# Optimization experiments

Measured on AMD Instinct MI355X. Metric: run time of the kernel, lower is better.

## Reference

```python
import jax, jax.numpy as jnp
import numpy as np

N_CLASSES = 100
MAX_POSSIBLE = 8.0
A, B, C_COEF = 1.0, 0.1, 0.0


def setup_inputs() -> dict:
    key = jax.random.key(0)
    k1, k2 = jax.random.split(key)
    pred = jax.random.normal(k1, (2000000, 64), dtype=jnp.float32)
    group_idx = jax.random.randint(k2, (2000000,), 0, N_CLASSES, dtype=jnp.int64)
    return {"pred": pred, "group_idx": group_idx}


def reference(pred, group_idx):
    C = N_CLASSES
    idx = group_idx.astype(jnp.int32)
    ones = jnp.ones((pred.shape[0],), dtype=pred.dtype)
    counts = jax.ops.segment_sum(ones, idx, num_segments=C)          # [C]
    s = jax.ops.segment_sum(pred, idx, num_segments=C)               # [C, D]
    sq = jax.ops.segment_sum(pred * pred, idx, num_segments=C)       # [C, D]
    cnt = counts[:, None]
    mean = s / cnt                                                   # [C, D]
    # unbiased variance (torch .std default ddof=1)
    var = (sq - cnt * mean * mean) / (cnt - 1.0)
    std = jnp.sqrt(jnp.maximum(var, 0.0))                            # [C, D]

    cov = jnp.sum(jnp.sum(std, axis=0) ** 2) / C

    # pairwise squared distances between class means, [C, C]
    gram = mean @ mean.T
    norms = jnp.diagonal(gram)
    dist = norms[:, None] + norms[None, :] - 2.0 * gram
    pair_mask = jnp.tril(jnp.ones((C, C), dtype=bool), k=-1)         # i > j pairs
    n_pairs = C * (C - 1) / 2.0
    mean_distance = jnp.sum(jnp.where(pair_mask, dist, 0.0)) / n_pairs
    min_dist = jnp.min(jnp.where(pair_mask, dist, jnp.inf))

    loss = (A * cov
            + B * (MAX_POSSIBLE - mean_distance) ** 2
            + C_COEF * (MAX_POSSIBLE - min_dist) ** 2)
    return (loss, mean_distance, min_dist, cov)
```

## Files before the change

### kernel.cpp

```cpp
#include <hip/hip_runtime.h>
#include <math.h>

#define NCLS 100
#define D 64
#define GACC_FLOATS (NCLS * D * 2 + NCLS)
#define G1 512
#define BLK 256
#define PBLK 12800
#define SUPF 8192

typedef __attribute__((ext_vector_type(8)))  short bf16x8;
typedef __attribute__((ext_vector_type(16))) float f32x16;

#define ZV16 {0.f,0.f,0.f,0.f,0.f,0.f,0.f,0.f,0.f,0.f,0.f,0.f,0.f,0.f,0.f,0.f}

union B8 { uint32_t u[4]; bf16x8 v; };

__device__ __forceinline__ uint32_t cvtpk(float lo, float hi) {
    uint32_t r;
    asm("v_cvt_pk_bf16_f32 %0, %1, %2" : "=v"(r) : "v"(lo), "v"(hi));
    return r;
}

__device__ __forceinline__ void global_fadd(float* p, float v) {
    asm volatile("global_atomic_add_f32 %0, %1, off"
                 :: "v"((uint64_t)(uintptr_t)p), "v"(v));
}

__device__ __forceinline__ void lds_fadd(uint32_t byteoff, float v) {
    asm volatile("ds_add_f32 %0, %1" :: "v"(byteoff), "v"(v));
}

struct IdxRegs { int4 a, b, c, d; };

__device__ __forceinline__ IdxRegs load_idx(const int* __restrict__ idx, size_t mtile, int kg) {
    const int* p = idx + mtile * 32 + (size_t)kg * 8;
    IdxRegs r;
    r.a = *(const int4*)p;        r.b = *(const int4*)(p + 4);
    r.c = *(const int4*)(p + 16); r.d = *(const int4*)(p + 20);
    return r;
}

__device__ __forceinline__ void stage_super(const float* __restrict__ pred, size_t st,
                                            float* buf, int w, int lane) {
    const float* src = pred + st * SUPF;
    #pragma unroll
    for (int r = 0; r < 8; ++r) {
        int c = r * 4 + w;
        const float* gs = src + (size_t)c * 256 + (size_t)lane * 4;
        float* ls = buf + c * 256;
        __builtin_amdgcn_global_load_lds(
            (const __attribute__((address_space(1))) uint32_t*)gs,
            (__attribute__((address_space(3))) uint32_t*)ls, 16, 0, 0);
    }
}

__global__ __launch_bounds__(BLK) void seg_mfma_kernel(
    const float* __restrict__ pred, const int* __restrict__ idx,
    float* __restrict__ part, float* __restrict__ gacc,
    int nrows, int atomicPath)
{
    __shared__ float sbuf[2][SUPF];

    const int bid   = blockIdx.x;
    const int tid   = threadIdx.x;
    const int lane  = tid & 63;
    const int w     = tid >> 6;
    const int col   = lane & 31;
    const int kg    = lane >> 5;
    const int mycls = w * 32 + col;

    f32x16 aS0 = ZV16, aS1 = ZV16, aQ0 = ZV16, aQ1 = ZV16;

    const size_t nst = (size_t)nrows >> 7;
    const size_t st0 = (size_t)bid * nst / G1;
    const size_t st1 = ((size_t)bid + 1) * nst / G1;

    if (st0 < st1) {
        stage_super(pred, st0, sbuf[0], w, lane);
        IdxRegs ir = load_idx(idx, st0 * 4, kg);
        __syncthreads();

        int cur = 0;
        for (size_t st = st0; st < st1; ++st) {
            if (st + 1 < st1)
                stage_super(pred, st + 1, sbuf[cur ^ 1], w, lane);

            #pragma unroll
            for (int mt = 0; mt < 4; ++mt) {
                size_t nmt = st * 4 + mt + 1;
                IdxRegs irn = (nmt < st1 * 4) ? load_idx(idx, nmt, kg) : ir;

                const float* pb = sbuf[cur] + mt * 2048;
                #pragma unroll
                for (int kk = 0; kk < 2; ++kk) {
                    const int4 i0 = kk ? ir.c : ir.a;
                    const int4 i1 = kk ? ir.d : ir.b;
                    B8 ab;
                    ab.u[0] = cvtpk(i0.x==mycls?1.f:0.f, i0.y==mycls?1.f:0.f);
                    ab.u[1] = cvtpk(i0.z==mycls?1.f:0.f, i0.w==mycls?1.f:0.f);
                    ab.u[2] = cvtpk(i1.x==mycls?1.f:0.f, i1.y==mycls?1.f:0.f);
                    ab.u[3] = cvtpk(i1.z==mycls?1.f:0.f, i1.w==mycls?1.f:0.f);

                    const float* base = pb + (kk * 16 + kg * 8) * 64 + col;
                    #pragma unroll
                    for (int n = 0; n < 2; ++n) {
                        float v[8];
                        #pragma unroll
                        for (int e = 0; e < 8; ++e) v[e] = base[e * 64 + n * 32];
                        B8 bv, bq;
                        #pragma unroll
                        for (int e = 0; e < 4; ++e) {
                            bv.u[e] = cvtpk(v[2*e],         v[2*e+1]);
                            bq.u[e] = cvtpk(v[2*e]*v[2*e],  v[2*e+1]*v[2*e+1]);
                        }
                        if (n == 0) {
                            aS0 = __builtin_amdgcn_mfma_f32_32x32x16_bf16(ab.v, bv.v, aS0, 0, 0, 0);
                            aQ0 = __builtin_amdgcn_mfma_f32_32x32x16_bf16(ab.v, bq.v, aQ0, 0, 0, 0);
                        } else {
                            aS1 = __builtin_amdgcn_mfma_f32_32x32x16_bf16(ab.v, bv.v, aS1, 0, 0, 0);
                            aQ1 = __builtin_amdgcn_mfma_f32_32x32x16_bf16(ab.v, bq.v, aQ1, 0, 0, 0);
                        }
                    }
                }
                ir = irn;
            }
            __syncthreads();
            cur ^= 1;
        }
    }

    if (bid == 0 && (nrows & 127)) {
        for (size_t base = nst * 128; base < (size_t)nrows; base += 16) {
            int c[8]; float v0[8], v1[8];
            #pragma unroll
            for (int e = 0; e < 8; ++e) {
                size_t kk = base + (size_t)kg * 8 + e;
                bool ok = kk < (size_t)nrows;
                c[e]  = ok ? idx[kk] : -1;
                v0[e] = ok ? pred[kk * 64 + col] : 0.0f;
                v1[e] = ok ? pred[kk * 64 + 32 + col] : 0.0f;
            }
            B8 ab, b0, q0, b1, q1;
            #pragma unroll
            for (int e = 0; e < 4; ++e) {
                ab.u[e] = cvtpk(c[2*e]==mycls?1.f:0.f, c[2*e+1]==mycls?1.f:0.f);
                b0.u[e] = cvtpk(v0[2*e],          v0[2*e+1]);
                q0.u[e] = cvtpk(v0[2*e]*v0[2*e],  v0[2*e+1]*v0[2*e+1]);
                b1.u[e] = cvtpk(v1[2*e],          v1[2*e+1]);
                q1.u[e] = cvtpk(v1[2*e]*v1[2*e],  v1[2*e+1]*v1[2*e+1]);
            }
            aS0 = __builtin_amdgcn_mfma_f32_32x32x16_bf16(ab.v, b0.v, aS0, 0, 0, 0);
            aQ0 = __builtin_amdgcn_mfma_f32_32x32x16_bf16(ab.v, q0.v, aQ0, 0, 0, 0);
            aS1 = __builtin_amdgcn_mfma_f32_32x32x16_bf16(ab.v, b1.v, aS1, 0, 0, 0);
            aQ1 = __builtin_amdgcn_mfma_f32_32x32x16_bf16(ab.v, q1.v, aQ1, 0, 0, 0);
        }
    }

    if (!atomicPath) {
        float* pp = part + (size_t)bid * PBLK;
        #pragma unroll
        for (int reg = 0; reg < 16; ++reg) {
            int row = (reg & 3) + 8 * (reg >> 2) + 4 * kg;
            int gm  = w * 32 + row;
            if (gm < NCLS) {
                pp[gm * 64 + col]              = aS0[reg];
                pp[gm * 64 + 32 + col]         = aS1[reg];
                pp[6400 + gm * 64 + col]       = aQ0[reg];
                pp[6400 + gm * 64 + 32 + col]  = aQ1[reg];
            }
        }
    } else {
        #pragma unroll
        for (int reg = 0; reg < 16; ++reg) {
            int row = (reg & 3) + 8 * (reg >> 2) + 4 * kg;
            int gm  = w * 32 + row;
            if (gm < NCLS) {
                global_fadd(&gacc[gm * 64 + col],             aS0[reg]);
                global_fadd(&gacc[gm * 64 + 32 + col],        aS1[reg]);
                global_fadd(&gacc[6400 + gm * 64 + col],      aQ0[reg]);
                global_fadd(&gacc[6400 + gm * 64 + 32 + col], aQ1[reg]);
            }
        }
    }
}

__global__ __launch_bounds__(256) void hist_kernel(
    const int* __restrict__ idx, float* __restrict__ gcnt, int nrows)
{
    __shared__ uint32_t hh[NCLS];
    for (int i = threadIdx.x; i < NCLS; i += 256) hh[i] = 0u;
    __syncthreads();

    const int tid = blockIdx.x * 256 + threadIdx.x;
    const int stride = gridDim.x * 256;
    const int n4 = nrows >> 2;
    for (int i = tid; i < n4; i += stride) {
        int4 c = ((const int4*)idx)[i];
        atomicAdd(&hh[c.x], 1u); atomicAdd(&hh[c.y], 1u);
        atomicAdd(&hh[c.z], 1u); atomicAdd(&hh[c.w], 1u);
    }
    for (int i = (n4 << 2) + tid; i < nrows; i += stride)
        atomicAdd(&hh[idx[i]], 1u);
    __syncthreads();

    for (int i = threadIdx.x; i < NCLS; i += 256)
        if (hh[i]) global_fadd(&gcnt[i], (float)hh[i]);
}

__global__ __launch_bounds__(256) void reduce_kernel(
    const float* __restrict__ part, float* __restrict__ gacc)
{
    int pos = blockIdx.x * 256 + threadIdx.x;
    if (pos >= PBLK) return;
    const int bq = G1 / 8;
    int b0 = blockIdx.y * bq;

    const float* p = part + (size_t)b0 * PBLK + pos;
    float s0 = 0.f, s1 = 0.f, s2 = 0.f, s3 = 0.f;
    #pragma unroll 1
    for (int b = 0; b + 4 <= bq; b += 4) {
        s0 += p[(size_t)(b + 0) * PBLK];
        s1 += p[(size_t)(b + 1) * PBLK];
        s2 += p[(size_t)(b + 2) * PBLK];
        s3 += p[(size_t)(b + 3) * PBLK];
    }
    global_fadd(&gacc[pos], (s0 + s1) + (s2 + s3));
}

#define MSTR 68

__global__ __launch_bounds__(1024) void finalize_kernel(
    const float* __restrict__ gacc, float* __restrict__ out)
{
    __shared__ float mean_s[NCLS * MSTR];
    __shared__ float colstd[D];
    __shared__ float norms[NCLS];
    __shared__ float redSum[16], redMin[16];
    __shared__ float s_cov;

    const float* gSum = gacc;
    const float* gSq  = gacc + NCLS * D;
    const float* gCnt = gacc + 2 * NCLS * D;

    for (int d = threadIdx.x; d < D; d += 1024) colstd[d] = 0.0f;
    __syncthreads();

    for (int i = threadIdx.x; i < NCLS * D; i += 1024) {
        int c = i >> 6, d = i & 63;
        float cnt = gCnt[c];
        float m   = gSum[i] / cnt;
        float var = (gSq[i] - cnt * m * m) / (cnt - 1.0f);
        float sd  = sqrtf(fmaxf(var, 0.0f));
        mean_s[c * MSTR + d] = m;
        lds_fadd((uint32_t)(uintptr_t)(&colstd[d]), sd);
    }
    asm volatile("s_waitcnt lgkmcnt(0)" ::: "memory");
    __syncthreads();

    if (threadIdx.x < 64) {
        float v = colstd[threadIdx.x];
        v = v * v;
        for (int o = 32; o; o >>= 1) v += __shfl_down(v, o);
        if (threadIdx.x == 0) s_cov = v / (float)NCLS;
    }

    for (int c = threadIdx.x; c < NCLS; c += 1024) {
        const float4* mp = (const float4*)&mean_s[c * MSTR];
        float n = 0.0f;
        #pragma unroll
        for (int d4 = 0; d4 < D / 4; ++d4) {
            float4 a = mp[d4];
            n += a.x * a.x + a.y * a.y + a.z * a.z + a.w * a.w;
        }
        norms[c] = n;
    }
    __syncthreads();

    const int n_pairs = NCLS * (NCLS - 1) / 2;
    float lsum = 0.0f, lmin = INFINITY;
    for (int p = threadIdx.x; p < n_pairs; p += 1024) {
        int i = (int)((1.0f + sqrtf(1.0f + 8.0f * (float)p)) * 0.5f);
        while (i * (i - 1) / 2 > p) --i;
        while ((i + 1) * i / 2 <= p) ++i;
        int j = p - i * (i - 1) / 2;

        const float4* mi = (const float4*)&mean_s[i * MSTR];
        const float4* mj = (const float4*)&mean_s[j * MSTR];
        float dot = 0.0f;
        #pragma unroll
        for (int d4 = 0; d4 < D / 4; ++d4) {
            float4 a = mi[d4], b = mj[d4];
            dot += a.x * b.x + a.y * b.y + a.z * b.z + a.w * b.w;
        }
        float dist = norms[i] + norms[j] - 2.0f * dot;
        lsum += dist;
        lmin = fminf(lmin, dist);
    }

    for (int o = 32; o; o >>= 1) {
        lsum += __shfl_down(lsum, o);
        lmin = fminf(lmin, __shfl_down(lmin, o));
    }
    int ww = threadIdx.x >> 6;
    if ((threadIdx.x & 63) == 0) { redSum[ww] = lsum; redMin[ww] = lmin; }
    __syncthreads();

    if (threadIdx.x == 0) {
        float S = 0.0f, M = INFINITY;
        for (int k = 0; k < 16; ++k) { S += redSum[k]; M = fminf(M, redMin[k]); }
        float md  = S / (float)n_pairs;
        float cov = s_cov;
        float e   = 8.0f - md;
        float loss = 1.0f * cov + 0.1f * e * e;
        out[0] = loss;
        out[1] = md;
        out[2] = M;
        out[3] = cov;
    }
}

extern "C" void kernel_launch(void* const* d_in, const int* in_sizes, int n_in,
                              void* d_out, int out_size, void* d_ws, size_t ws_size,
                              hipStream_t stream) {
    const float* pred = (const float*)d_in[0];
    const int*   gidx = (const int*)d_in[1];
    float* out = (float*)d_out;
    int nrows = in_sizes[1];

    const size_t partFloats = (size_t)G1 * PBLK;

    if (ws_size >= (partFloats + GACC_FLOATS) * sizeof(float)) {
        float* part = (float*)d_ws;
        float* gacc = part + partFloats;
        hipMemsetAsync(gacc, 0, GACC_FLOATS * sizeof(float), stream);
        seg_mfma_kernel<<<G1, BLK, 0, stream>>>(pred, gidx, part, gacc, nrows, 0);
        hist_kernel<<<1024, 256, 0, stream>>>(gidx, gacc + 2 * NCLS * D, nrows);
        dim3 gridR((PBLK + 255) / 256, 8);
        reduce_kernel<<<gridR, 256, 0, stream>>>(part, gacc);
        finalize_kernel<<<1, 1024, 0, stream>>>(gacc, out);
    } else {
        float* gacc = (float*)d_ws;
        hipMemsetAsync(gacc, 0, GACC_FLOATS * sizeof(float), stream);
        seg_mfma_kernel<<<G1, BLK, 0, stream>>>(pred, gidx, nullptr, gacc, nrows, 1);
        hist_kernel<<<1024, 256, 0, stream>>>(gidx, gacc + 2 * NCLS * D, nrows);
        finalize_kernel<<<1, 1024, 0, stream>>>(gacc, out);
    }
}
```

Before: 189.0 us.

## Stage indices through LDS and hand-schedule async loads with explicit waitcnt

Group-index loads move from per-thread global reads into the same async global-to-LDS staging path as pred. The main loop uses explicit vmcnt waits, raw s_barrier and inline-asm ds_read2/ds_read_b128 fetches. The super-tile is halved and the grid doubled, with launch bounds of four blocks per CU, so more blocks stay resident while memory traffic overlaps with MFMA work. The vmcnt(5) count assumes exactly five outstanding loads per stage and the asm LDS addressing is hand-computed, so any mismatch in either would silently corrupt results.

```diff
diff --git a/kernel.cpp b/kernel.cpp
--- a/kernel.cpp
+++ b/kernel.cpp
@@ -4,13 +4,15 @@
 #define NCLS 100
 #define D 64
 #define GACC_FLOATS (NCLS * D * 2 + NCLS)
-#define G1 512
+#define G1 1024
 #define BLK 256
 #define PBLK 12800
-#define SUPF 8192
+#define SUPF 4096
 
 typedef __attribute__((ext_vector_type(8)))  short bf16x8;
 typedef __attribute__((ext_vector_type(16))) float f32x16;
+typedef __attribute__((ext_vector_type(2)))  float f32x2;
+typedef __attribute__((ext_vector_type(4)))  int   i32x4;
 
 #define ZV16 {0.f,0.f,0.f,0.f,0.f,0.f,0.f,0.f,0.f,0.f,0.f,0.f,0.f,0.f,0.f,0.f}
 
@@ -31,36 +33,32 @@
     asm volatile("ds_add_f32 %0, %1" :: "v"(byteoff), "v"(v));
 }
 
-struct IdxRegs { int4 a, b, c, d; };
-
-__device__ __forceinline__ IdxRegs load_idx(const int* __restrict__ idx, size_t mtile, int kg) {
-    const int* p = idx + mtile * 32 + (size_t)kg * 8;
-    IdxRegs r;
-    r.a = *(const int4*)p;        r.b = *(const int4*)(p + 4);
-    r.c = *(const int4*)(p + 16); r.d = *(const int4*)(p + 20);
-    return r;
-}
-
-__device__ __forceinline__ void stage_super(const float* __restrict__ pred, size_t st,
-                                            float* buf, int w, int lane) {
+__device__ __forceinline__ void stage_super(const float* __restrict__ pred,
+                                            const int* __restrict__ idx, size_t st,
+                                            float* sb, int* ib, int w, int lane) {
     const float* src = pred + st * SUPF;
     #pragma unroll
-    for (int r = 0; r < 8; ++r) {
+    for (int r = 0; r < 4; ++r) {
         int c = r * 4 + w;
         const float* gs = src + (size_t)c * 256 + (size_t)lane * 4;
-        float* ls = buf + c * 256;
+        float* ls = sb + c * 256;
         __builtin_amdgcn_global_load_lds(
             (const __attribute__((address_space(1))) uint32_t*)gs,
             (__attribute__((address_space(3))) uint32_t*)ls, 16, 0, 0);
     }
-}
-
-__global__ __launch_bounds__(BLK) void seg_mfma_kernel(
+    const int* gi = idx + st * 64 + lane;
+    __builtin_amdgcn_global_load_lds(
+        (const __attribute__((address_space(1))) uint32_t*)gi,
+        (__attribute__((address_space(3))) uint32_t*)ib, 4, 0, 0);
+}
+
+__global__ __launch_bounds__(BLK, 4) void seg_mfma_kernel(
     const float* __restrict__ pred, const int* __restrict__ idx,
     float* __restrict__ part, float* __restrict__ gacc,
     int nrows, int atomicPath)
 {
     __shared__ float sbuf[2][SUPF];
+    __shared__ int   ibuf[2][64];
 
     const int bid   = blockIdx.x;
     const int tid   = threadIdx.x;
@@ -72,66 +70,79 @@
 
     f32x16 aS0 = ZV16, aS1 = ZV16, aQ0 = ZV16, aQ1 = ZV16;
 
-    const size_t nst = (size_t)nrows >> 7;
+    const size_t nst = (size_t)nrows >> 6;
     const size_t st0 = (size_t)bid * nst / G1;
     const size_t st1 = ((size_t)bid + 1) * nst / G1;
 
     if (st0 < st1) {
-        stage_super(pred, st0, sbuf[0], w, lane);
-        IdxRegs ir = load_idx(idx, st0 * 4, kg);
-        __syncthreads();
+        stage_super(pred, idx, st0, sbuf[0], ibuf[0], w, lane);
 
         int cur = 0;
         for (size_t st = st0; st < st1; ++st) {
-            if (st + 1 < st1)
-                stage_super(pred, st + 1, sbuf[cur ^ 1], w, lane);
+            if (st + 1 < st1) {
+                stage_super(pred, idx, st + 1, sbuf[cur ^ 1], ibuf[cur ^ 1], w, lane);
+                asm volatile("s_waitcnt vmcnt(5)" ::: "memory");
+            } else {
+                asm volatile("s_waitcnt vmcnt(0)" ::: "memory");
+            }
+            __builtin_amdgcn_sched_barrier(0);
+            __builtin_amdgcn_s_barrier();
+
+            const uint32_t sb32 = (uint32_t)(uintptr_t)&sbuf[cur][0];
+            const uint32_t ib32 = (uint32_t)(uintptr_t)&ibuf[cur][0];
 
             #pragma unroll
-            for (int mt = 0; mt < 4; ++mt) {
-                size_t nmt = st * 4 + mt + 1;
-                IdxRegs irn = (nmt < st1 * 4) ? load_idx(idx, nmt, kg) : ir;
-
-                const float* pb = sbuf[cur] + mt * 2048;
+            for (int mt = 0; mt < 2; ++mt) {
                 #pragma unroll
                 for (int kk = 0; kk < 2; ++kk) {
-                    const int4 i0 = kk ? ir.c : ir.a;
-                    const int4 i1 = kk ? ir.d : ir.b;
+                    const int rowk = mt * 32 + kk * 16 + kg * 8;
+                    const uint32_t ia = ib32 + (uint32_t)(rowk * 4);
+                    const uint32_t b0 = sb32 + (uint32_t)(rowk * 256) + (uint32_t)col * 4;
+
+                    i32x4 q0, q1;
+                    f32x2 p0, p1, p2, p3, p4, p5, p6, p7;
+                    asm volatile("ds_read_b128 %0, %1"            : "=v"(q0) : "v"(ia));
+                    asm volatile("ds_read_b128 %0, %1 offset:16"  : "=v"(q1) : "v"(ia));
+                    asm volatile("ds_read2_b32 %0, %1 offset0:0 offset1:64"     : "=v"(p0) : "v"(b0));
+                    asm volatile("ds_read2_b32 %0, %1 offset0:128 offset1:192"  : "=v"(p1) : "v"(b0));
+                    asm volatile("ds_read2_b32 %0, %1 offset0:0 offset1:64"     : "=v"(p2) : "v"(b0 + 1024u));
+                    asm volatile("ds_read2_b32 %0, %1 offset0:128 offset1:192"  : "=v"(p3) : "v"(b0 + 1024u));
+                    asm volatile("ds_read2_b32 %0, %1 offset0:0 offset1:64"     : "=v"(p4) : "v"(b0 + 128u));
+                    asm volatile("ds_read2_b32 %0, %1 offset0:128 offset1:192"  : "=v"(p5) : "v"(b0 + 128u));
+                    asm volatile("ds_read2_b32 %0, %1 offset0:0 offset1:64"     : "=v"(p6) : "v"(b0 + 1152u));
+                    asm volatile("ds_read2_b32 %0, %1 offset0:128 offset1:192"  : "=v"(p7) : "v"(b0 + 1152u));
+                    asm volatile("s_waitcnt lgkmcnt(0)" ::: "memory");
+                    __builtin_amdgcn_sched_barrier(0);
+
                     B8 ab;
-                    ab.u[0] = cvtpk(i0.x==mycls?1.f:0.f, i0.y==mycls?1.f:0.f);
-                    ab.u[1] = cvtpk(i0.z==mycls?1.f:0.f, i0.w==mycls?1.f:0.f);
-                    ab.u[2] = cvtpk(i1.x==mycls?1.f:0.f, i1.y==mycls?1.f:0.f);
-                    ab.u[3] = cvtpk(i1.z==mycls?1.f:0.f, i1.w==mycls?1.f:0.f);
-
-                    const float* base = pb + (kk * 16 + kg * 8) * 64 + col;
-                    #pragma unroll
-                    for (int n = 0; n < 2; ++n) {
-                        float v[8];
-                        #pragma unroll
-                        for (int e = 0; e < 8; ++e) v[e] = base[e * 64 + n * 32];
-                        B8 bv, bq;
-                        #pragma unroll
-                        for (int e = 0; e < 4; ++e) {
-                            bv.u[e] = cvtpk(v[2*e],         v[2*e+1]);
-                            bq.u[e] = cvtpk(v[2*e]*v[2*e],  v[2*e+1]*v[2*e+1]);
-                        }
-                        if (n == 0) {
-                            aS0 = __builtin_amdgcn_mfma_f32_32x32x16_bf16(ab.v, bv.v, aS0, 0, 0, 0);
-                            aQ0 = __builtin_amdgcn_mfma_f32_32x32x16_bf16(ab.v, bq.v, aQ0, 0, 0, 0);
-                        } else {
-                            aS1 = __builtin_amdgcn_mfma_f32_32x32x16_bf16(ab.v, bv.v, aS1, 0, 0, 0);
-                            aQ1 = __builtin_amdgcn_mfma_f32_32x32x16_bf16(ab.v, bq.v, aQ1, 0, 0, 0);
-                        }
-                    }
+                    ab.u[0] = cvtpk(q0.x==mycls?1.f:0.f, q0.y==mycls?1.f:0.f);
+                    ab.u[1] = cvtpk(q0.z==mycls?1.f:0.f, q0.w==mycls?1.f:0.f);
+                    ab.u[2] = cvtpk(q1.x==mycls?1.f:0.f, q1.y==mycls?1.f:0.f);
+                    ab.u[3] = cvtpk(q1.z==mycls?1.f:0.f, q1.w==mycls?1.f:0.f);
+
+                    B8 bv, bq;
+                    bv.u[0] = cvtpk(p0.x, p0.y);  bq.u[0] = cvtpk(p0.x*p0.x, p0.y*p0.y);
+                    bv.u[1] = cvtpk(p1.x, p1.y);  bq.u[1] = cvtpk(p1.x*p1.x, p1.y*p1.y);
+                    bv.u[2] = cvtpk(p2.x, p2.y);  bq.u[2] = cvtpk(p2.x*p2.x, p2.y*p2.y);
+                    bv.u[3] = cvtpk(p3.x, p3.y);  bq.u[3] = cvtpk(p3.x*p3.x, p3.y*p3.y);
+                    aS0 = __builtin_amdgcn_mfma_f32_32x32x16_bf16(ab.v, bv.v, aS0, 0, 0, 0);
+                    aQ0 = __builtin_amdgcn_mfma_f32_32x32x16_bf16(ab.v, bq.v, aQ0, 0, 0, 0);
+
+                    bv.u[0] = cvtpk(p4.x, p4.y);  bq.u[0] = cvtpk(p4.x*p4.x, p4.y*p4.y);
+                    bv.u[1] = cvtpk(p5.x, p5.y);  bq.u[1] = cvtpk(p5.x*p5.x, p5.y*p5.y);
+                    bv.u[2] = cvtpk(p6.x, p6.y);  bq.u[2] = cvtpk(p6.x*p6.x, p6.y*p6.y);
+                    bv.u[3] = cvtpk(p7.x, p7.y);  bq.u[3] = cvtpk(p7.x*p7.x, p7.y*p7.y);
+                    aS1 = __builtin_amdgcn_mfma_f32_32x32x16_bf16(ab.v, bv.v, aS1, 0, 0, 0);
+                    aQ1 = __builtin_amdgcn_mfma_f32_32x32x16_bf16(ab.v, bq.v, aQ1, 0, 0, 0);
                 }
-                ir = irn;
-            }
-            __syncthreads();
+            }
+            __builtin_amdgcn_s_barrier();
             cur ^= 1;
         }
     }
 
-    if (bid == 0 && (nrows & 127)) {
-        for (size_t base = nst * 128; base < (size_t)nrows; base += 16) {
+    if (bid == 0 && (nrows & 63)) {
+        for (size_t base = nst * 64; base < (size_t)nrows; base += 16) {
             int c[8]; float v0[8], v1[8];
             #pragma unroll
             for (int e = 0; e < 8; ++e) {
```

Result: faster. 174.8 us (-7.5%).
